# Performance work log

Hardware: AMD Instinct MI355X
Metric: run time of the kernel (lower is better)

The kernel has to match this reference:

```python
import jax, jax.numpy as jnp
import numpy as np

N_T = 2_000_000      # terrain nodes
E_SEQ = 2_000_000    # sequence edges
E_AS = 2_000_000     # assignment edges
N_TOR = 1_000_000    # torus nodes
E_TR = 8_000_000     # transport edges
TD, OD, PD, N_OPS = 4, 3, 1, 4  # terrain dim, torus dim, polarity dim, num operators


def setup_inputs() -> dict:
    key = jax.random.key(0)
    ks = jax.random.split(key, 12)
    inp = {
        "x_terrain": jax.random.normal(ks[0], (N_T, TD), jnp.float32),
        "polarity": jax.random.normal(ks[1], (E_AS, PD), jnp.float32),
        "x_torus": jax.random.normal(ks[2], (N_TOR, OD), jnp.float32),
        "seq_ei": jax.random.randint(ks[3], (2, E_SEQ), 0, N_T),
        "assign_src": jax.random.randint(ks[4], (E_AS,), 0, N_T),
        "assign_dst": jax.random.randint(ks[5], (E_AS,), 0, N_OPS),
        "tr_ei": jax.random.randint(ks[6], (2, E_TR), 0, N_TOR),
        # learned params (nn.Linear convention: y = x @ W.T + b)
        "W_seq": jax.random.normal(ks[7], (TD, TD), jnp.float32) * 0.5,      # SequenceConv.lin, no bias
        "op_W": jax.random.normal(ks[8], (N_OPS, TD, TD + PD), jnp.float32) * 0.4,
        "op_b": jax.random.normal(ks[9], (N_OPS, TD), jnp.float32) * 0.1,
        "gate_W": jax.random.normal(ks[10], (2 * OD, 1), jnp.float32) * 0.4,  # TransportConv.gate
        "gate_b": jax.random.normal(ks[11], (1,), jnp.float32) * 0.1,
    }
    return inp


def _engine_fwd(x_terrain, polarity, x_torus, W_seq, op_W, op_b, gate_W, gate_b,
                seq_ei, assign_src, assign_dst, tr_ei):
    # 1) SequenceConv: add-aggregated linear message along terrain cycle, residual add
    msg = x_terrain[seq_ei[0]] @ W_seq.T                       # [E_seq, TD]
    agg = jnp.zeros_like(x_terrain).at[seq_ei[1]].add(msg)     # scatter-add to dst
    x_t = x_terrain + agg

    # 2) per-node operator transform: first assignment edge per source node
    E = assign_src.shape[0]
    pos = jnp.arange(E, dtype=jnp.int32)
    first = jax.ops.segment_min(pos, assign_src, num_segments=x_t.shape[0])  # fill = int32 max
    has = first < E                                            # nodes with >=1 assignment
    fe = jnp.clip(first, 0, E - 1)
    op_idx = jnp.clip(assign_dst[fe], 0, op_W.shape[0] - 1)    # [N_T]
    pol = polarity[fe]                                         # [N_T, 1]
    inp = jnp.concatenate([x_t, pol], axis=-1)                 # [N_T, TD+1]
    out = jnp.einsum('nij,nj->ni', op_W[op_idx], inp) + op_b[op_idx]
    x_t = jnp.where(has[:, None], out, x_t)

    # 3) TransportConv: sigmoid-gated mean aggregation over torus edges, residual add
    src, dst = tr_ei[0], tr_ei[1]
    xi, xj = x_torus[dst], x_torus[src]
    gate = jax.nn.sigmoid(jnp.concatenate([xi, xj], axis=-1) @ gate_W + gate_b)  # [E_tr,1]
    m = gate * xj
    s = jax.ops.segment_sum(m, dst, num_segments=x_torus.shape[0])
    cnt = jax.ops.segment_sum(jnp.ones((m.shape[0],), m.dtype), dst,
                              num_segments=x_torus.shape[0])
    x_tor = x_torus + s / jnp.maximum(cnt, 1.0)[:, None]
    return x_t, x_tor


def reference(x_terrain, polarity, x_torus, seq_ei, assign_src, assign_dst, tr_ei,
              W_seq, op_W, op_b, gate_W, gate_b):
    return _engine_fwd(x_terrain, polarity, x_torus, W_seq, op_W, op_b, gate_W, gate_b,
                       seq_ei, assign_src, assign_dst, tr_ei)
```

## Files before the change

### kernel.cpp

```cpp
#include <hip/hip_runtime.h>
#include <hip/hip_fp16.h>
#include <math.h>

#define N_T   2000000
#define E_SEQ 2000000
#define E_AS  2000000
#define N_TOR 1000000
#define E_TR  8000000

typedef unsigned long long u64;

__device__ __forceinline__ long long center_field(u64 t, int bits) {
    long long h = 1LL << (bits - 1);
    return (long long)((t & ((1ULL << bits) - 1)) ^ (u64)h) - h;
}

#define INIT_U64S ((size_t)N_T * 2 + N_TOR)
__global__ __launch_bounds__(256) void init_kernel(ulonglong2* __restrict__ ws) {
    size_t i = (size_t)blockIdx.x * blockDim.x + threadIdx.x;
    if (i >= INIT_U64S / 2) return;
    size_t idx64 = i * 2;
    u64 v = (idx64 >= (size_t)N_T && idx64 < (size_t)2 * N_T) ? ~0ULL : 0ULL;
    ws[i] = make_ulonglong2(v, v);
}

__global__ __launch_bounds__(256) void edge_kernel(
        const float* __restrict__ x_torus,
        const int* __restrict__ tr_src,
        const int* __restrict__ tr_dst,
        const float* __restrict__ gate_W,
        const float* __restrict__ gate_b,
        u64* __restrict__ tor_pk,
        const float4* __restrict__ x_terrain,
        const int* __restrict__ seq_src,
        const int* __restrict__ seq_dst,
        const float* __restrict__ W_seq,
        u64* __restrict__ agg_pk,
        const int* __restrict__ assign_src,
        const int* __restrict__ assign_dst,
        const float* __restrict__ polarity,
        u64* __restrict__ first_pk) {
    int i = blockIdx.x * blockDim.x + threadIdx.x;
    if (i < E_TR) {
        int e = i;
        int si = tr_src[e];
        int di = tr_dst[e];
        const float* xi = x_torus + (size_t)di * 3;
        const float* xj = x_torus + (size_t)si * 3;
        float xj0 = xj[0], xj1 = xj[1], xj2 = xj[2];
        float z = fmaf(xi[0], gate_W[0],
                  fmaf(xi[1], gate_W[1],
                  fmaf(xi[2], gate_W[2],
                  fmaf(xj0,  gate_W[3],
                  fmaf(xj1,  gate_W[4],
                  fmaf(xj2,  gate_W[5], gate_b[0]))))));
        float g = 1.0f / (1.0f + __expf(-z));
        long long f0 = __float2int_rn(g * xj0 * 128.0f);
        long long f1 = __float2int_rn(g * xj1 * 128.0f);
        long long f2 = __float2int_rn(g * xj2 * 128.0f);
        long long pk = f0 + (f1 << 17) + (f2 << 34) + (1LL << 51);
        atomicAdd(&tor_pk[di], (u64)pk);
    } else if (i < E_TR + E_SEQ) {
        int e = i - E_TR;
        int s = seq_src[e];
        int d = seq_dst[e];
        float4 x = x_terrain[s];
        float m0 = fmaf(x.x, W_seq[0],  fmaf(x.y, W_seq[1],  fmaf(x.z, W_seq[2],  x.w * W_seq[3])));
        float m1 = fmaf(x.x, W_seq[4],  fmaf(x.y, W_seq[5],  fmaf(x.z, W_seq[6],  x.w * W_seq[7])));
        float m2 = fmaf(x.x, W_seq[8],  fmaf(x.y, W_seq[9],  fmaf(x.z, W_seq[10], x.w * W_seq[11])));
        float m3 = fmaf(x.x, W_seq[12], fmaf(x.y, W_seq[13], fmaf(x.z, W_seq[14], x.w * W_seq[15])));
        long long f0 = __float2int_rn(m0 * 256.0f);
        long long f1 = __float2int_rn(m1 * 256.0f);
        long long f2 = __float2int_rn(m2 * 256.0f);
        long long f3 = __float2int_rn(m3 * 256.0f);
        long long pk = f0 + (f1 << 16) + (f2 << 32) + (f3 << 48);
        atomicAdd(&agg_pk[d], (u64)pk);
    } else if (i < E_TR + E_SEQ + E_AS) {
        int e = i - (E_TR + E_SEQ);
        int op = assign_dst[e] & 3;
        __half h = __float2half(polarity[e]);
        unsigned short hb;
        __builtin_memcpy(&hb, &h, 2);
        u64 key = ((u64)e << 18) | ((u64)op << 16) | (u64)hb;
        atomicMin(&first_pk[assign_src[e]], key);
    }
}

__global__ __launch_bounds__(256) void node_kernel(
        const float4* __restrict__ x_terrain,
        const u64* __restrict__ agg_pk,
        const u64* __restrict__ first_pk,
        const float* __restrict__ op_W,
        const float* __restrict__ op_b,
        float4* __restrict__ out_xt,
        const float* __restrict__ x_torus,
        const u64* __restrict__ tor_pk,
        float* __restrict__ out_tor) {
    int i = blockIdx.x * blockDim.x + threadIdx.x;
    if (i < N_T) {
        int n = i;
        float4 x = x_terrain[n];
        u64 t = agg_pk[n];
        long long m0 = center_field(t, 16); t = (t - (u64)m0) >> 16;
        long long m1 = center_field(t, 16); t = (t - (u64)m1) >> 16;
        long long m2 = center_field(t, 16); t = (t - (u64)m2) >> 16;
        long long m3 = center_field(t, 16);
        const float inv = 1.0f / 256.0f;
        x.x += (float)m0 * inv; x.y += (float)m1 * inv;
        x.z += (float)m2 * inv; x.w += (float)m3 * inv;
        u64 fp = first_pk[n];
        if ((fp >> 18) < (u64)E_AS) {
            int op = (int)((fp >> 16) & 3);
            unsigned short hb = (unsigned short)(fp & 0xFFFF);
            __half h;
            __builtin_memcpy(&h, &hb, 2);
            float pol = __half2float(h);
            const float* W = op_W + op * 20;
            const float* b = op_b + op * 4;
            float4 o;
            o.x = fmaf(x.x, W[0],  fmaf(x.y, W[1],  fmaf(x.z, W[2],  fmaf(x.w, W[3],  fmaf(pol, W[4],  b[0])))));
            o.y = fmaf(x.x, W[5],  fmaf(x.y, W[6],  fmaf(x.z, W[7],  fmaf(x.w, W[8],  fmaf(pol, W[9],  b[1])))));
            o.z = fmaf(x.x, W[10], fmaf(x.y, W[11], fmaf(x.z, W[12], fmaf(x.w, W[13], fmaf(pol, W[14], b[2])))));
            o.w = fmaf(x.x, W[15], fmaf(x.y, W[16], fmaf(x.z, W[17], fmaf(x.w, W[18], fmaf(pol, W[19], b[3])))));
            x = o;
        }
        out_xt[n] = x;
    } else if (i < N_T + N_TOR) {
        int n = i - N_T;
        u64 t = tor_pk[n];
        long long m0 = center_field(t, 17); t = (t - (u64)m0) >> 17;
        long long m1 = center_field(t, 17); t = (t - (u64)m1) >> 17;
        long long m2 = center_field(t, 17); t = (t - (u64)m2) >> 17;
        float cnt = (float)(t & 0x1FFF);
        float inv = (1.0f / 128.0f) / fmaxf(cnt, 1.0f);
        size_t b = (size_t)n * 3;
        out_tor[b + 0] = x_torus[b + 0] + (float)m0 * inv;
        out_tor[b + 1] = x_torus[b + 1] + (float)m1 * inv;
        out_tor[b + 2] = x_torus[b + 2] + (float)m2 * inv;
    }
}

extern "C" void kernel_launch(void* const* d_in, const int* in_sizes, int n_in,
                              void* d_out, int out_size, void* d_ws, size_t ws_size,
                              hipStream_t stream) {
    const float* x_terrain  = (const float*)d_in[0];
    const float* polarity   = (const float*)d_in[1];
    const float* x_torus    = (const float*)d_in[2];
    const int*   seq_ei     = (const int*)  d_in[3];
    const int*   assign_src = (const int*)  d_in[4];
    const int*   assign_dst = (const int*)  d_in[5];
    const int*   tr_ei      = (const int*)  d_in[6];
    const float* W_seq      = (const float*)d_in[7];
    const float* op_W       = (const float*)d_in[8];
    const float* op_b       = (const float*)d_in[9];
    const float* gate_W     = (const float*)d_in[10];
    const float* gate_b     = (const float*)d_in[11];

    float* out_xt  = (float*)d_out;
    float* out_tor = (float*)d_out + (size_t)N_T * 4;

    char* ws = (char*)d_ws;
    u64* agg_pk   = (u64*)ws;
    u64* first_pk = agg_pk + N_T;
    u64* tor_pk   = first_pk + N_T;

    const int B = 256;
    const long long init_v2 = (long long)(INIT_U64S / 2);
    init_kernel<<<(int)((init_v2 + B - 1) / B), B, 0, stream>>>((ulonglong2*)ws);

    const long long total_e = (long long)E_TR + E_SEQ + E_AS;
    edge_kernel<<<(int)((total_e + B - 1) / B), B, 0, stream>>>(
        x_torus, tr_ei, tr_ei + E_TR, gate_W, gate_b, tor_pk,
        (const float4*)x_terrain, seq_ei, seq_ei + E_SEQ, W_seq, agg_pk,
        assign_src, assign_dst, polarity, first_pk);
    const long long total_n = (long long)N_T + N_TOR;
    node_kernel<<<(int)((total_n + B - 1) / B), B, 0, stream>>>(
        (const float4*)x_terrain, agg_pk, first_pk, op_W, op_b, (float4*)out_xt,
        x_torus, tor_pk, out_tor);
}
```

Measured before the change: 686.8 us.

## Precompute per-node gate projections into padded float4 table before edge pass

Result: no change. 700.1 us (+1.9%).

```diff
diff --git a/kernel.cpp b/kernel.cpp
--- a/kernel.cpp
+++ b/kernel.cpp
@@ -24,12 +24,27 @@
     ws[i] = make_ulonglong2(v, v);
 }
 
+__global__ __launch_bounds__(256) void prep_kernel(
+        const float* __restrict__ x_torus,
+        const float* __restrict__ gate_W,
+        const float* __restrict__ gate_b,
+        float4* __restrict__ src_f4,
+        float* __restrict__ yi_arr) {
+    int n = blockIdx.x * blockDim.x + threadIdx.x;
+    if (n >= N_TOR) return;
+    const float* x = x_torus + (size_t)n * 3;
+    float x0 = x[0], x1 = x[1], x2 = x[2];
+    float yi = fmaf(x0, gate_W[0], fmaf(x1, gate_W[1], x2 * gate_W[2]));
+    float yj = fmaf(x0, gate_W[3], fmaf(x1, gate_W[4], fmaf(x2, gate_W[5], gate_b[0])));
+    src_f4[n] = make_float4(x0, x1, x2, yj);
+    yi_arr[n] = yi;
+}
+
 __global__ __launch_bounds__(256) void edge_kernel(
-        const float* __restrict__ x_torus,
+        const float4* __restrict__ src_f4,
+        const float* __restrict__ yi_arr,
         const int* __restrict__ tr_src,
         const int* __restrict__ tr_dst,
-        const float* __restrict__ gate_W,
-        const float* __restrict__ gate_b,
         u64* __restrict__ tor_pk,
         const float4* __restrict__ x_terrain,
         const int* __restrict__ seq_src,
@@ -43,27 +58,20 @@
     int i = blockIdx.x * blockDim.x + threadIdx.x;
     if (i < E_TR) {
         int e = i;
-        int si = tr_src[e];
-        int di = tr_dst[e];
-        const float* xi = x_torus + (size_t)di * 3;
-        const float* xj = x_torus + (size_t)si * 3;
-        float xj0 = xj[0], xj1 = xj[1], xj2 = xj[2];
-        float z = fmaf(xi[0], gate_W[0],
-                  fmaf(xi[1], gate_W[1],
-                  fmaf(xi[2], gate_W[2],
-                  fmaf(xj0,  gate_W[3],
-                  fmaf(xj1,  gate_W[4],
-                  fmaf(xj2,  gate_W[5], gate_b[0]))))));
+        int si = __builtin_nontemporal_load(tr_src + e);
+        int di = __builtin_nontemporal_load(tr_dst + e);
+        float4 s = src_f4[si];
+        float z = yi_arr[di] + s.w;
         float g = 1.0f / (1.0f + __expf(-z));
-        long long f0 = __float2int_rn(g * xj0 * 128.0f);
-        long long f1 = __float2int_rn(g * xj1 * 128.0f);
-        long long f2 = __float2int_rn(g * xj2 * 128.0f);
+        long long f0 = __float2int_rn(g * s.x * 128.0f);
+        long long f1 = __float2int_rn(g * s.y * 128.0f);
+        long long f2 = __float2int_rn(g * s.z * 128.0f);
         long long pk = f0 + (f1 << 17) + (f2 << 34) + (1LL << 51);
         atomicAdd(&tor_pk[di], (u64)pk);
     } else if (i < E_TR + E_SEQ) {
         int e = i - E_TR;
-        int s = seq_src[e];
-        int d = seq_dst[e];
+        int s = __builtin_nontemporal_load(seq_src + e);
+        int d = __builtin_nontemporal_load(seq_dst + e);
         float4 x = x_terrain[s];
         float m0 = fmaf(x.x, W_seq[0],  fmaf(x.y, W_seq[1],  fmaf(x.z, W_seq[2],  x.w * W_seq[3])));
         float m1 = fmaf(x.x, W_seq[4],  fmaf(x.y, W_seq[5],  fmaf(x.z, W_seq[6],  x.w * W_seq[7])));
@@ -77,12 +85,12 @@
         atomicAdd(&agg_pk[d], (u64)pk);
     } else if (i < E_TR + E_SEQ + E_AS) {
         int e = i - (E_TR + E_SEQ);
-        int op = assign_dst[e] & 3;
-        __half h = __float2half(polarity[e]);
+        int op = __builtin_nontemporal_load(assign_dst + e) & 3;
+        __half h = __float2half(__builtin_nontemporal_load(polarity + e));
         unsigned short hb;
         __builtin_memcpy(&hb, &h, 2);
         u64 key = ((u64)e << 18) | ((u64)op << 16) | (u64)hb;
-        atomicMin(&first_pk[assign_src[e]], key);
+        atomicMin(&first_pk[__builtin_nontemporal_load(assign_src + e)], key);
     }
 }
 
@@ -164,13 +172,18 @@
     u64* first_pk = agg_pk + N_T;
     u64* tor_pk   = first_pk + N_T;
 
+    float4* src_f4 = (float4*)d_out;
+    float*  yi_arr = (float*)d_out + (size_t)N_TOR * 4;
+
     const int B = 256;
     const long long init_v2 = (long long)(INIT_U64S / 2);
     init_kernel<<<(int)((init_v2 + B - 1) / B), B, 0, stream>>>((ulonglong2*)ws);
+    prep_kernel<<<(N_TOR + B - 1) / B, B, 0, stream>>>(x_torus, gate_W, gate_b,
+                                                       src_f4, yi_arr);
 
     const long long total_e = (long long)E_TR + E_SEQ + E_AS;
     edge_kernel<<<(int)((total_e + B - 1) / B), B, 0, stream>>>(
-        x_torus, tr_ei, tr_ei + E_TR, gate_W, gate_b, tor_pk,
+        src_f4, yi_arr, tr_ei, tr_ei + E_TR, tor_pk,
         (const float4*)x_terrain, seq_ei, seq_ei + E_SEQ, W_seq, agg_pk,
         assign_src, assign_dst, polarity, first_pk);
     const long long total_n = (long long)N_T + N_TOR;
```
